# Kernel tuning notes

Measured on AMD Instinct MI355X. Metric: run time of the kernel, lower is better.

## Reference

```python
import jax, jax.numpy as jnp
import numpy as np

MAX_IT = 20
LAMBDA_ROF = 7.0
SIGMA = 1.0 / (7.0 * 0.01)
TAU = 0.01
THETA = 0.5
M, N = 4096, 4096


def _forward_weighted_gradient(x, w):
    # x: [1, M, N], w: [2, M, N] -> [2, M, N]
    x0 = x[0]
    gx = jnp.pad(x0[:, 1:] - x0[:, :-1], ((0, 0), (0, 1)))  # last col stays 0
    gy = jnp.pad(x0[1:, :] - x0[:-1, :], ((0, 1), (0, 0)))  # last row stays 0
    return jnp.stack([gx, gy]) * w


def _backward_weighted_divergence(y, w):
    # y, w: [2, M, N] -> [1, M, N]
    yw = w * y
    h, v = yw[0], yw[1]
    d_h = jnp.concatenate([h[:, :1], h[:, 1:-1] - h[:, :-2], -h[:, -2:-1]], axis=1)
    d_v = jnp.concatenate([v[:1, :], v[1:-1, :] - v[:-2, :], -v[-2:-1, :]], axis=0)
    return (d_h + d_v)[None]


def setup_inputs() -> dict:
    key = jax.random.key(0)
    k1, k2, k3 = jax.random.split(key, 3)
    img_obs = jax.random.uniform(k1, (1, M, N), dtype=jnp.float32)
    w = jax.random.uniform(k2, (2, M, N), dtype=jnp.float32)
    y0 = jax.random.uniform(k3, (2, M, N), dtype=jnp.float32)
    return {"img_obs": img_obs, "w": w, "y0": y0}


def reference(img_obs, w, y0):
    denom = 1.0 + LAMBDA_ROF * TAU

    def body(carry, _):
        x, x_tilde, y = carry
        # dual update + L-inf ball projection (prox == clip to [-1, 1])
        y = jnp.clip(y + SIGMA * _forward_weighted_gradient(x_tilde, w), -1.0, 1.0)
        x_old = x
        # primal update
        x = (x + TAU * _backward_weighted_divergence(y, w)
             + LAMBDA_ROF * TAU * img_obs) / denom
        # over-relaxation
        x_tilde = x + THETA * (x - x_old)
        return (x, x_tilde, y), None

    (x, x_tilde, y), _ = jax.lax.scan(body, (img_obs, img_obs, y0), None, length=MAX_IT)
    return x_tilde
```

## Files before the change

### kernel.cpp

```cpp
#include <hip/hip_runtime.h>


#define MM 4096
#define NN 4096
static constexpr size_t PP = (size_t)MM * NN;

static constexpr float SIGMA_F  = 14.285714285714286f;
static constexpr float TAU_F    = 0.01f;
static constexpr float THETA_F  = 0.5f;
static constexpr float LT_F     = 0.07f;
static constexpr float INV_DEN  = 1.0f / 1.07f;

typedef _Float16 h16;
typedef __attribute__((ext_vector_type(8))) _Float16 h16x8;
typedef __attribute__((ext_vector_type(4))) float f32x4;

__device__ __forceinline__ float clip1(float v) {
    return fminf(1.0f, fmaxf(-1.0f, v));
}

template<bool H>
__device__ __forceinline__ void ld8(const void* p, size_t idx, float* o) {
    if constexpr (H) {
        h16x8 v = *reinterpret_cast<const h16x8*>(reinterpret_cast<const h16*>(p) + idx);
        for (int e = 0; e < 8; ++e) o[e] = (float)v[e];
    } else {
        const float* q = reinterpret_cast<const float*>(p) + idx;
        f32x4 a = *reinterpret_cast<const f32x4*>(q);
        f32x4 b = *reinterpret_cast<const f32x4*>(q + 4);
        o[0]=a.x; o[1]=a.y; o[2]=a.z; o[3]=a.w;
        o[4]=b.x; o[5]=b.y; o[6]=b.z; o[7]=b.w;
    }
}
template<bool H>
__device__ __forceinline__ float ld1(const void* p, size_t idx) {
    if constexpr (H) return (float)reinterpret_cast<const h16*>(p)[idx];
    else             return reinterpret_cast<const float*>(p)[idx];
}

template<int XM, bool LAST, bool WH>
__global__ __launch_bounds__(256)
void fused_kernel(const void* __restrict__ xprev, const void* __restrict__ xcur,
                  const h16* __restrict__ yin, const void* __restrict__ w,
                  const float* __restrict__ img,
                  h16* __restrict__ xnext, h16* __restrict__ yout,
                  float* __restrict__ out)
{
    constexpr bool HP = (XM == 2);
    constexpr bool HC = (XM >= 1);
    const int i  = blockIdx.y * 4 + threadIdx.y;
    const int j0 = (blockIdx.x * 64 + threadIdx.x) * 8;
    const size_t idx = (size_t)i * NN + j0;
    const bool hasL = (j0 > 0);
    const bool hasR = (j0 + 8 < NN);
    const bool hasU = (i > 0);
    const bool hasD = (i < MM - 1);

    float xpC[8], xcC[8], xtC[8];
    ld8<HP>(xprev, idx, xpC);
    ld8<HC>(xcur,  idx, xcC);
    for (int e = 0; e < 8; ++e) xtC[e] = fmaf(THETA_F, xcC[e] - xpC[e], xcC[e]);

    float xtL = 0.f, xtR = 0.f;
    if (hasL) { float xp = ld1<HP>(xprev, idx-1), xc = ld1<HC>(xcur, idx-1);
                xtL = fmaf(THETA_F, xc - xp, xc); }
    if (hasR) { float xp = ld1<HP>(xprev, idx+8), xc = ld1<HC>(xcur, idx+8);
                xtR = fmaf(THETA_F, xc - xp, xc); }

    float xtU[8], xtD[8];
    if (hasU) {
        float xp[8], xc[8];
        ld8<HP>(xprev, idx - NN, xp);
        ld8<HC>(xcur,  idx - NN, xc);
        for (int e = 0; e < 8; ++e) xtU[e] = fmaf(THETA_F, xc[e] - xp[e], xc[e]);
    } else {
        for (int e = 0; e < 8; ++e) xtU[e] = 0.f;
    }
    if (hasD) {
        float xp[8], xc[8];
        ld8<HP>(xprev, idx + NN, xp);
        ld8<HC>(xcur,  idx + NN, xc);
        for (int e = 0; e < 8; ++e) xtD[e] = fmaf(THETA_F, xc[e] - xp[e], xc[e]);
    } else {
        for (int e = 0; e < 8; ++e) xtD[e] = 0.f;
    }

    float y0C[8], y1C[8], y1U[8];
    ld8<true>(yin, idx, y0C);
    ld8<true>(yin, PP + idx, y1C);
    float y0L = hasL ? ld1<true>(yin, idx - 1) : 0.f;
    if (hasU) {
        ld8<true>(yin, PP + idx - NN, y1U);
    } else {
        for (int e = 0; e < 8; ++e) y1U[e] = 0.f;
    }

    float w0C[8], w1C[8], w1U[8];
    ld8<WH>(w, idx, w0C);
    ld8<WH>(w, PP + idx, w1C);
    float w0L = hasL ? ld1<WH>(w, idx - 1) : 0.f;
    if (hasU) {
        ld8<WH>(w, PP + idx - NN, w1U);
    } else {
        for (int e = 0; e < 8; ++e) w1U[e] = 0.f;
    }

    float gv[8];
    ld8<false>(img, idx, gv);

    float y0n[8];
    for (int e = 0; e < 7; ++e)
        y0n[e] = clip1(fmaf(SIGMA_F * (xtC[e+1] - xtC[e]), w0C[e], y0C[e]));
    { float gx7 = hasR ? (xtR - xtC[7]) : 0.f;
      y0n[7] = clip1(fmaf(SIGMA_F * gx7, w0C[7], y0C[7])); }
    float y0nL = hasL ? clip1(fmaf(SIGMA_F * (xtC[0] - xtL), w0L, y0L)) : 0.f;

    float y1nC[8], y1nU[8];
    for (int e = 0; e < 8; ++e) {
        float gy = hasD ? (xtD[e] - xtC[e]) : 0.f;
        y1nC[e] = clip1(fmaf(SIGMA_F * gy, w1C[e], y1C[e]));
    }
    if (hasU) {
        for (int e = 0; e < 8; ++e)
            y1nU[e] = clip1(fmaf(SIGMA_F * (xtC[e] - xtU[e]), w1U[e], y1U[e]));
    } else {
        for (int e = 0; e < 8; ++e) y1nU[e] = 0.f;
    }

    float h[8];
    for (int e = 0; e < 8; ++e) h[e] = w0C[e] * y0n[e];
    const float hL = hasL ? w0L * y0nL : 0.f;
    float dh[8];
    dh[0] = h[0] - hL;
    for (int e = 1; e < 7; ++e) dh[e] = h[e] - h[e-1];
    dh[7] = (hasR ? h[7] : 0.f) - h[6];

    float dv[8];
    for (int e = 0; e < 8; ++e)
        dv[e] = (hasD ? w1C[e] * y1nC[e] : 0.f) - (hasU ? w1U[e] * y1nU[e] : 0.f);

    float xn[8];
    for (int e = 0; e < 8; ++e)
        xn[e] = (xcC[e] + TAU_F * (dh[e] + dv[e]) + LT_F * gv[e]) * INV_DEN;

    if constexpr (!LAST) {
        h16x8 s0, s1, sx;
        for (int e = 0; e < 8; ++e) {
            s0[e] = (h16)y0n[e];
            s1[e] = (h16)y1nC[e];
            sx[e] = (h16)xn[e];
        }
        *reinterpret_cast<h16x8*>(yout + idx)      = s0;
        *reinterpret_cast<h16x8*>(yout + PP + idx) = s1;
        *reinterpret_cast<h16x8*>(xnext + idx)     = sx;
    } else {
        float xt_[8];
        for (int e = 0; e < 8; ++e) xt_[e] = fmaf(THETA_F, xn[e] - xcC[e], xn[e]);
        f32x4 a, b;
        a.x = xt_[0]; a.y = xt_[1]; a.z = xt_[2]; a.w = xt_[3];
        b.x = xt_[4]; b.y = xt_[5]; b.z = xt_[6]; b.w = xt_[7];
        *reinterpret_cast<f32x4*>(out + idx)     = a;
        *reinterpret_cast<f32x4*>(out + idx + 4) = b;
    }
}

__global__ __launch_bounds__(256)
void cvt_f32_h16(const float* __restrict__ src, h16* __restrict__ dst) {
    const size_t t = (size_t)blockIdx.x * blockDim.x + threadIdx.x;
    const size_t idx = t * 8;
    f32x4 a = *reinterpret_cast<const f32x4*>(src + idx);
    f32x4 b = *reinterpret_cast<const f32x4*>(src + idx + 4);
    h16x8 v;
    v[0]=(h16)a.x; v[1]=(h16)a.y; v[2]=(h16)a.z; v[3]=(h16)a.w;
    v[4]=(h16)b.x; v[5]=(h16)b.y; v[6]=(h16)b.z; v[7]=(h16)b.w;
    *reinterpret_cast<h16x8*>(dst + idx) = v;
}

template<int XM, bool LAST>
static void launch_one(bool wh, dim3 g, dim3 b, hipStream_t s,
                       const void* xp, const void* xc, const h16* yin, const void* w,
                       const float* img, h16* xn, h16* yo, float* out) {
    if (wh) fused_kernel<XM, LAST, true ><<<g, b, 0, s>>>(xp, xc, yin, w, img, xn, yo, out);
    else    fused_kernel<XM, LAST, false><<<g, b, 0, s>>>(xp, xc, yin, w, img, xn, yo, out);
}

extern "C" void kernel_launch(void* const* d_in, const int* in_sizes, int n_in,
                              void* d_out, int out_size, void* d_ws, size_t ws_size,
                              hipStream_t stream) {
    const float* img = (const float*)d_in[0];
    const float* w   = (const float*)d_in[1];
    const float* y0  = (const float*)d_in[2];

    h16* base = (h16*)d_ws;
    h16* xb[3] = { base, base + PP, base + 2 * PP };
    h16* yA  = base + 3 * PP;
    h16* w_h = base + 5 * PP;
    h16* yB  = (h16*)d_out;

    const bool use_wh = (ws_size >= 7 * PP * sizeof(h16));

    {
        const int blocks = (int)(2 * PP / (8 * 256));
        cvt_f32_h16<<<blocks, 256, 0, stream>>>(y0, yB);
        if (use_wh) cvt_f32_h16<<<blocks, 256, 0, stream>>>(w, w_h);
    }
    const void* wp = use_wh ? (const void*)w_h : (const void*)w;

    const dim3 block(64, 4);
    const dim3 grid(NN / (64 * 8), MM / 4);
    const int MAX_IT = 20;

    for (int t = 0; t < MAX_IT; ++t) {
        const void* xp = (t <= 1) ? (const void*)img : (const void*)xb[(t - 2) % 3];
        const void* xc = (t == 0) ? (const void*)img : (const void*)xb[(t - 1) % 3];
        const h16* yin = (t % 2 == 0) ? yB : yA;
        h16* yout      = (t % 2 == 0) ? yA : yB;
        h16* xnext     = xb[t % 3];
        const bool last = (t == MAX_IT - 1);

        if (t == 0)
            launch_one<0, false>(use_wh, grid, block, stream, xp, xc, yin, wp, img, xnext, yout, (float*)d_out);
        else if (t == 1)
            launch_one<1, false>(use_wh, grid, block, stream, xp, xc, yin, wp, img, xnext, yout, (float*)d_out);
        else if (!last)
            launch_one<2, false>(use_wh, grid, block, stream, xp, xc, yin, wp, img, xnext, yout, (float*)d_out);
        else
            launch_one<2, true >(use_wh, grid, block, stream, xp, xc, yin, wp, img, xnext, yout, (float*)d_out);
    }
}
```

Measured before the change: 1.746 ms.

## Fuse two PDHG iterations per launch with shared-memory halo tiles

Replaces the one-iteration-per-launch stencil with a temporally blocked kernel. Each launch runs two primal-dual iterations on a 16x128 tile plus halo held in LDS, so the launch count drops from 20 to 10 and intermediate x/y traffic to global memory is roughly halved. The fp16 conversions of y0, w and img move into the first launch, and img can now be stored in fp16. Halo rows and columns are recomputed redundantly, and the larger LDS footprint and extra barriers may limit occupancy.

After: 1.706 ms. 1.02x faster.

```diff
diff --git a/kernel.cpp b/kernel.cpp
--- a/kernel.cpp
+++ b/kernel.cpp
@@ -15,173 +15,359 @@
 typedef __attribute__((ext_vector_type(8))) _Float16 h16x8;
 typedef __attribute__((ext_vector_type(4))) float f32x4;
 
+#define TR 16
+#define TC 128
+#define BR 20
+#define NSTRIP 18
+#define LSW 152
+
 __device__ __forceinline__ float clip1(float v) {
     return fminf(1.0f, fmaxf(-1.0f, v));
 }
 
 template<bool H>
-__device__ __forceinline__ void ld8(const void* p, size_t idx, float* o) {
+__device__ __forceinline__ void gld8(const void* __restrict__ p, long idx, bool ok, float* o) {
+    if (!ok) {
+        #pragma unroll
+        for (int e = 0; e < 8; ++e) o[e] = 0.f;
+        return;
+    }
     if constexpr (H) {
         h16x8 v = *reinterpret_cast<const h16x8*>(reinterpret_cast<const h16*>(p) + idx);
+        #pragma unroll
         for (int e = 0; e < 8; ++e) o[e] = (float)v[e];
     } else {
         const float* q = reinterpret_cast<const float*>(p) + idx;
         f32x4 a = *reinterpret_cast<const f32x4*>(q);
         f32x4 b = *reinterpret_cast<const f32x4*>(q + 4);
-        o[0]=a.x; o[1]=a.y; o[2]=a.z; o[3]=a.w;
-        o[4]=b.x; o[5]=b.y; o[6]=b.z; o[7]=b.w;
-    }
-}
+        o[0]=a.x;o[1]=a.y;o[2]=a.z;o[3]=a.w;o[4]=b.x;o[5]=b.y;o[6]=b.z;o[7]=b.w;
+    }
+}
+
 template<bool H>
-__device__ __forceinline__ float ld1(const void* p, size_t idx) {
+__device__ __forceinline__ float gld1(const void* __restrict__ p, long idx, bool ok) {
+    if (!ok) return 0.f;
     if constexpr (H) return (float)reinterpret_cast<const h16*>(p)[idx];
     else             return reinterpret_cast<const float*>(p)[idx];
 }
 
-template<int XM, bool LAST, bool WH>
-__global__ __launch_bounds__(256)
-void fused_kernel(const void* __restrict__ xprev, const void* __restrict__ xcur,
-                  const h16* __restrict__ yin, const void* __restrict__ w,
-                  const float* __restrict__ img,
-                  h16* __restrict__ xnext, h16* __restrict__ yout,
-                  float* __restrict__ out)
+__device__ __forceinline__ void lds8h(const h16* p, float* o) {
+    h16x8 v = *reinterpret_cast<const h16x8*>(p);
+    #pragma unroll
+    for (int e = 0; e < 8; ++e) o[e] = (float)v[e];
+}
+__device__ __forceinline__ void lds8f(const float* p, float* o) {
+    f32x4 a = *reinterpret_cast<const f32x4*>(p);
+    f32x4 b = *reinterpret_cast<const f32x4*>(p + 4);
+    o[0]=a.x;o[1]=a.y;o[2]=a.z;o[3]=a.w;o[4]=b.x;o[5]=b.y;o[6]=b.z;o[7]=b.w;
+}
+
+template<int MODE, bool WH, bool IH>
+__global__ __launch_bounds__(256, 4)
+void pd2(const h16* __restrict__ xprev, const h16* __restrict__ xcur,
+         const void* __restrict__ yin, const void* __restrict__ w,
+         const void* __restrict__ img,
+         h16* __restrict__ xo1, h16* __restrict__ xo2, h16* __restrict__ yo,
+         h16* __restrict__ w_h, h16* __restrict__ img_h,
+         float* __restrict__ out)
 {
-    constexpr bool HP = (XM == 2);
-    constexpr bool HC = (XM >= 1);
-    const int i  = blockIdx.y * 4 + threadIdx.y;
-    const int j0 = (blockIdx.x * 64 + threadIdx.x) * 8;
-    const size_t idx = (size_t)i * NN + j0;
-    const bool hasL = (j0 > 0);
-    const bool hasR = (j0 + 8 < NN);
-    const bool hasU = (i > 0);
-    const bool hasD = (i < MM - 1);
-
-    float xpC[8], xcC[8], xtC[8];
-    ld8<HP>(xprev, idx, xpC);
-    ld8<HC>(xcur,  idx, xcC);
-    for (int e = 0; e < 8; ++e) xtC[e] = fmaf(THETA_F, xcC[e] - xpC[e], xcC[e]);
-
-    float xtL = 0.f, xtR = 0.f;
-    if (hasL) { float xp = ld1<HP>(xprev, idx-1), xc = ld1<HC>(xcur, idx-1);
-                xtL = fmaf(THETA_F, xc - xp, xc); }
-    if (hasR) { float xp = ld1<HP>(xprev, idx+8), xc = ld1<HC>(xcur, idx+8);
-                xtR = fmaf(THETA_F, xc - xp, xc); }
-
-    float xtU[8], xtD[8];
-    if (hasU) {
-        float xp[8], xc[8];
-        ld8<HP>(xprev, idx - NN, xp);
-        ld8<HC>(xcur,  idx - NN, xc);
-        for (int e = 0; e < 8; ++e) xtU[e] = fmaf(THETA_F, xc[e] - xp[e], xc[e]);
-    } else {
-        for (int e = 0; e < 8; ++e) xtU[e] = 0.f;
-    }
-    if (hasD) {
-        float xp[8], xc[8];
-        ld8<HP>(xprev, idx + NN, xp);
-        ld8<HC>(xcur,  idx + NN, xc);
-        for (int e = 0; e < 8; ++e) xtD[e] = fmaf(THETA_F, xc[e] - xp[e], xc[e]);
-    } else {
-        for (int e = 0; e < 8; ++e) xtD[e] = 0.f;
-    }
-
-    float y0C[8], y1C[8], y1U[8];
-    ld8<true>(yin, idx, y0C);
-    ld8<true>(yin, PP + idx, y1C);
-    float y0L = hasL ? ld1<true>(yin, idx - 1) : 0.f;
-    if (hasU) {
-        ld8<true>(yin, PP + idx - NN, y1U);
-    } else {
-        for (int e = 0; e < 8; ++e) y1U[e] = 0.f;
-    }
-
-    float w0C[8], w1C[8], w1U[8];
-    ld8<WH>(w, idx, w0C);
-    ld8<WH>(w, PP + idx, w1C);
-    float w0L = hasL ? ld1<WH>(w, idx - 1) : 0.f;
-    if (hasU) {
-        ld8<WH>(w, PP + idx - NN, w1U);
-    } else {
-        for (int e = 0; e < 8; ++e) w1U[e] = 0.f;
-    }
-
-    float gv[8];
-    ld8<false>(img, idx, gv);
-
-    float y0n[8];
-    for (int e = 0; e < 7; ++e)
-        y0n[e] = clip1(fmaf(SIGMA_F * (xtC[e+1] - xtC[e]), w0C[e], y0C[e]));
-    { float gx7 = hasR ? (xtR - xtC[7]) : 0.f;
-      y0n[7] = clip1(fmaf(SIGMA_F * gx7, w0C[7], y0C[7])); }
-    float y0nL = hasL ? clip1(fmaf(SIGMA_F * (xtC[0] - xtL), w0L, y0L)) : 0.f;
-
-    float y1nC[8], y1nU[8];
-    for (int e = 0; e < 8; ++e) {
-        float gy = hasD ? (xtD[e] - xtC[e]) : 0.f;
-        y1nC[e] = clip1(fmaf(SIGMA_F * gy, w1C[e], y1C[e]));
-    }
-    if (hasU) {
-        for (int e = 0; e < 8; ++e)
-            y1nU[e] = clip1(fmaf(SIGMA_F * (xtC[e] - xtU[e]), w1U[e], y1U[e]));
-    } else {
-        for (int e = 0; e < 8; ++e) y1nU[e] = 0.f;
-    }
-
-    float h[8];
-    for (int e = 0; e < 8; ++e) h[e] = w0C[e] * y0n[e];
-    const float hL = hasL ? w0L * y0nL : 0.f;
-    float dh[8];
-    dh[0] = h[0] - hL;
-    for (int e = 1; e < 7; ++e) dh[e] = h[e] - h[e-1];
-    dh[7] = (hasR ? h[7] : 0.f) - h[6];
-
-    float dv[8];
-    for (int e = 0; e < 8; ++e)
-        dv[e] = (hasD ? w1C[e] * y1nC[e] : 0.f) - (hasU ? w1U[e] * y1nU[e] : 0.f);
-
-    float xn[8];
-    for (int e = 0; e < 8; ++e)
-        xn[e] = (xcC[e] + TAU_F * (dh[e] + dv[e]) + LT_F * gv[e]) * INV_DEN;
-
-    if constexpr (!LAST) {
-        h16x8 s0, s1, sx;
-        for (int e = 0; e < 8; ++e) {
-            s0[e] = (h16)y0n[e];
-            s1[e] = (h16)y1nC[e];
-            sx[e] = (h16)xn[e];
-        }
-        *reinterpret_cast<h16x8*>(yout + idx)      = s0;
-        *reinterpret_cast<h16x8*>(yout + PP + idx) = s1;
-        *reinterpret_cast<h16x8*>(xnext + idx)     = sx;
-    } else {
-        float xt_[8];
-        for (int e = 0; e < 8; ++e) xt_[e] = fmaf(THETA_F, xn[e] - xcC[e], xn[e]);
-        f32x4 a, b;
-        a.x = xt_[0]; a.y = xt_[1]; a.z = xt_[2]; a.w = xt_[3];
-        b.x = xt_[4]; b.y = xt_[5]; b.z = xt_[6]; b.w = xt_[7];
-        *reinterpret_cast<f32x4*>(out + idx)     = a;
-        *reinterpret_cast<f32x4*>(out + idx + 4) = b;
-    }
-}
-
-__global__ __launch_bounds__(256)
-void cvt_f32_h16(const float* __restrict__ src, h16* __restrict__ dst) {
-    const size_t t = (size_t)blockIdx.x * blockDim.x + threadIdx.x;
-    const size_t idx = t * 8;
-    f32x4 a = *reinterpret_cast<const f32x4*>(src + idx);
-    f32x4 b = *reinterpret_cast<const f32x4*>(src + idx + 4);
-    h16x8 v;
-    v[0]=(h16)a.x; v[1]=(h16)a.y; v[2]=(h16)a.z; v[3]=(h16)a.w;
-    v[4]=(h16)b.x; v[5]=(h16)b.y; v[6]=(h16)b.z; v[7]=(h16)b.w;
-    *reinterpret_cast<h16x8*>(dst + idx) = v;
-}
-
-template<int XM, bool LAST>
-static void launch_one(bool wh, dim3 g, dim3 b, hipStream_t s,
-                       const void* xp, const void* xc, const h16* yin, const void* w,
-                       const float* img, h16* xn, h16* yo, float* out) {
-    if (wh) fused_kernel<XM, LAST, true ><<<g, b, 0, s>>>(xp, xc, yin, w, img, xn, yo, out);
-    else    fused_kernel<XM, LAST, false><<<g, b, 0, s>>>(xp, xc, yin, w, img, xn, yo, out);
+    constexpr bool FIRST = (MODE == 0);
+    constexpr bool LAST  = (MODE == 2);
+    constexpr bool WRH = (!FIRST) && WH;
+    constexpr bool IRH = (!FIRST) && IH;
+
+    __shared__ float sXT[BR][LSW];
+    __shared__ h16   sX [BR][LSW];
+    __shared__ h16   sY0[BR][LSW];
+    __shared__ h16   sY1[BR][LSW];
+
+    const int tid = threadIdx.x;
+    const int bi0 = blockIdx.y * TR;
+    const int bj0 = blockIdx.x * TC;
+
+    for (int t = tid; t < BR * NSTRIP; t += 256) {
+        const int r = t / NSTRIP, s = t - r * NSTRIP;
+        const int gi = bi0 - 2 + r;
+        const int gj = bj0 - 8 + 8 * s;
+        const long idx = (long)gi * NN + gj;
+        const bool ok = (gi >= 0) & (gi < MM) & (gj >= 0) & (gj < NN);
+        const int l = 8 * s;
+        float xt8[8]; h16x8 xh;
+        if constexpr (FIRST) {
+            float v[8];
+            gld8<false>(img, idx, ok, v);
+            #pragma unroll
+            for (int e = 0; e < 8; ++e) { xt8[e] = v[e]; xh[e] = (h16)v[e]; }
+        } else {
+            float xp[8], xc[8];
+            gld8<true>(xprev, idx, ok, xp);
+            gld8<true>(xcur,  idx, ok, xc);
+            #pragma unroll
+            for (int e = 0; e < 8; ++e) {
+                xt8[e] = fmaf(THETA_F, xc[e] - xp[e], xc[e]);
+                xh[e]  = (h16)xc[e];
+            }
+        }
+        #pragma unroll
+        for (int e = 0; e < 8; ++e) sXT[r][l + e] = xt8[e];
+        *reinterpret_cast<h16x8*>(&sX[r][l]) = xh;
+    }
+    __syncthreads();
+
+    for (int t = tid; t < 19 * NSTRIP; t += 256) {
+        const int r = t / NSTRIP, s = t - r * NSTRIP;
+        const int gi = bi0 - 2 + r;
+        const int gj0 = bj0 - 8 + 8 * s;
+        const long idx = (long)gi * NN + gj0;
+        const bool ok = (gi >= 0) & (gi < MM) & (gj0 >= 0) & (gj0 < NN);
+        const int l = 8 * s;
+
+        float y0v[8], y1v[8], w0v[8], w1v[8];
+        gld8<!FIRST>(yin, idx, ok, y0v);
+        gld8<!FIRST>(yin, (long)PP + idx, ok, y1v);
+        gld8<WRH>(w, idx, ok, w0v);
+        gld8<WRH>(w, (long)PP + idx, ok, w1v);
+
+        float xtC[8], xtD[8];
+        lds8f(&sXT[r][l], xtC);
+        const float xtR = sXT[r][l + 8];
+        lds8f(&sXT[r + 1][l], xtD);
+
+        h16x8 y0s, y1s;
+        #pragma unroll
+        for (int e = 0; e < 8; ++e) {
+            const int gj = gj0 + e;
+            const float xtr = (e < 7) ? xtC[e + 1] : xtR;
+            const float gx = (gj < NN - 1) ? (xtr - xtC[e]) : 0.f;
+            const float gy = (gi < MM - 1) ? (xtD[e] - xtC[e]) : 0.f;
+            y0s[e] = (h16)clip1(fmaf(SIGMA_F * gx, w0v[e], y0v[e]));
+            y1s[e] = (h16)clip1(fmaf(SIGMA_F * gy, w1v[e], y1v[e]));
+        }
+        *reinterpret_cast<h16x8*>(&sY0[r][l]) = y0s;
+        *reinterpret_cast<h16x8*>(&sY1[r][l]) = y1s;
+
+        if constexpr (FIRST && WH) {
+            if (r >= 2 && r <= 17 && s >= 1 && s <= 16) {
+                h16x8 a, b;
+                #pragma unroll
+                for (int e = 0; e < 8; ++e) { a[e] = (h16)w0v[e]; b[e] = (h16)w1v[e]; }
+                *reinterpret_cast<h16x8*>(&w_h[idx]) = a;
+                *reinterpret_cast<h16x8*>(&w_h[PP + idx]) = b;
+            }
+        }
+    }
+    __syncthreads();
+
+    for (int t = tid; t < 18 * NSTRIP; t += 256) {
+        const int r = 1 + t / NSTRIP, s = t % NSTRIP;
+        const int gi = bi0 - 2 + r;
+        const int gj0 = bj0 - 8 + 8 * s;
+        const long idx = (long)gi * NN + gj0;
+        const bool ok  = (gi >= 0) & (gi < MM) & (gj0 >= 0) & (gj0 < NN);
+        const bool okU = (gi >= 1) & (gj0 >= 0) & (gj0 < NN);
+        const int l = 8 * s;
+
+        float y0C[8], y1C[8], y1U[8];
+        lds8h(&sY0[r][l], y0C);
+        lds8h(&sY1[r][l], y1C);
+        lds8h(&sY1[r - 1][l], y1U);
+        const int lm1 = (l > 0) ? (l - 1) : 0;
+        const float y0L = (float)sY0[r][lm1];
+
+        float w0C[8], w1C[8], w1U[8];
+        gld8<WRH>(w, idx, ok, w0C);
+        gld8<WRH>(w, (long)PP + idx, ok, w1C);
+        gld8<WRH>(w, (long)PP + idx - NN, okU, w1U);
+        const float w0L = gld1<WRH>(w, idx - 1, ok & (gj0 > 0));
+
+        float gim[8];
+        gld8<IRH>(img, idx, ok, gim);
+
+        float xc[8];
+        if constexpr (FIRST) {
+            #pragma unroll
+            for (int e = 0; e < 8; ++e) xc[e] = gim[e];
+        } else {
+            lds8h(&sX[r][l], xc);
+        }
+
+        float h[8];
+        #pragma unroll
+        for (int e = 0; e < 8; ++e) {
+            const int gj = gj0 + e;
+            h[e] = (gj < NN - 1) ? w0C[e] * y0C[e] : 0.f;
+        }
+        const float hL = w0L * y0L;
+        float dh[8];
+        dh[0] = h[0] - hL;
+        #pragma unroll
+        for (int e = 1; e < 8; ++e) dh[e] = h[e] - h[e - 1];
+
+        const bool notbot = (gi < MM - 1);
+        h16x8 xh; float xt1[8];
+        #pragma unroll
+        for (int e = 0; e < 8; ++e) {
+            const float vC = notbot ? w1C[e] * y1C[e] : 0.f;
+            const float vU = w1U[e] * y1U[e];
+            const float xv = (xc[e] + TAU_F * (dh[e] + vC - vU) + LT_F * gim[e]) * INV_DEN;
+            const h16 hh = (h16)xv;
+            const float xvh = (float)hh;
+            xh[e] = hh;
+            xt1[e] = fmaf(THETA_F, xvh - xc[e], xvh);
+        }
+        *reinterpret_cast<h16x8*>(&sX[r][l]) = xh;
+        #pragma unroll
+        for (int e = 0; e < 8; ++e) sXT[r][l + e] = xt1[e];
+
+        if constexpr (!LAST) {
+            if (r >= 2 && r <= 17 && s >= 1 && s <= 16)
+                *reinterpret_cast<h16x8*>(&xo1[idx]) = xh;
+        }
+        if constexpr (FIRST && IH) {
+            if (r >= 2 && r <= 17 && s >= 1 && s <= 16) {
+                h16x8 g8;
+                #pragma unroll
+                for (int e = 0; e < 8; ++e) g8[e] = (h16)gim[e];
+                *reinterpret_cast<h16x8*>(&img_h[idx]) = g8;
+            }
+        }
+    }
+    __syncthreads();
+
+    for (int t = tid; t < 17 * 17; t += 256) {
+        const int r = 1 + t / 17, s = t % 17;
+        const int gi = bi0 - 2 + r;
+        const int gj0 = bj0 - 8 + 8 * s;
+        const long idx = (long)gi * NN + gj0;
+        const bool ok = (gi >= 0) & (gi < MM) & (gj0 >= 0) & (gj0 < NN);
+        const int l = 8 * s;
+
+        float w0v[8], w1v[8];
+        gld8<WRH>(w, idx, ok, w0v);
+        gld8<WRH>(w, (long)PP + idx, ok, w1v);
+
+        float xtC[8], xtD[8];
+        lds8f(&sXT[r][l], xtC);
+        const float xtR = sXT[r][l + 8];
+        lds8f(&sXT[r + 1][l], xtD);
+
+        float y0p[8], y1p[8];
+        lds8h(&sY0[r][l], y0p);
+        lds8h(&sY1[r][l], y1p);
+
+        h16x8 y0s, y1s;
+        #pragma unroll
+        for (int e = 0; e < 8; ++e) {
+            const int gj = gj0 + e;
+            const float xtr = (e < 7) ? xtC[e + 1] : xtR;
+            const float gx = (gj < NN - 1) ? (xtr - xtC[e]) : 0.f;
+            const float gy = (gi < MM - 1) ? (xtD[e] - xtC[e]) : 0.f;
+            y0s[e] = (h16)clip1(fmaf(SIGMA_F * gx, w0v[e], y0p[e]));
+            y1s[e] = (h16)clip1(fmaf(SIGMA_F * gy, w1v[e], y1p[e]));
+        }
+        *reinterpret_cast<h16x8*>(&sY0[r][l]) = y0s;
+        *reinterpret_cast<h16x8*>(&sY1[r][l]) = y1s;
+        if constexpr (!LAST) {
+            if (r >= 2 && s >= 1) {
+                *reinterpret_cast<h16x8*>(&yo[idx]) = y0s;
+                *reinterpret_cast<h16x8*>(&yo[PP + idx]) = y1s;
+            }
+        }
+    }
+    __syncthreads();
+
+    {
+        const int r = 2 + (tid >> 4);
+        const int s = 1 + (tid & 15);
+        const int gi = bi0 - 2 + r;
+        const int gj0 = bj0 - 8 + 8 * s;
+        const long idx = (long)gi * NN + gj0;
+        const int l = 8 * s;
+
+        float y0C[8], y1C[8], y1U[8];
+        lds8h(&sY0[r][l], y0C);
+        lds8h(&sY1[r][l], y1C);
+        lds8h(&sY1[r - 1][l], y1U);
+        const float y0L = (float)sY0[r][l - 1];
+
+        float w0C[8], w1C[8], w1U[8];
+        gld8<WRH>(w, idx, true, w0C);
+        gld8<WRH>(w, (long)PP + idx, true, w1C);
+        gld8<WRH>(w, (long)PP + idx - NN, gi > 0, w1U);
+        const float w0L = gld1<WRH>(w, idx - 1, gj0 > 0);
+
+        float gim[8];
+        gld8<IRH>(img, idx, true, gim);
+
+        float xc1[8];
+        lds8h(&sX[r][l], xc1);
+
+        float h[8];
+        #pragma unroll
+        for (int e = 0; e < 8; ++e) {
+            const int gj = gj0 + e;
+            h[e] = (gj < NN - 1) ? w0C[e] * y0C[e] : 0.f;
+        }
+        const float hL = w0L * y0L;
+        float dh[8];
+        dh[0] = h[0] - hL;
+        #pragma unroll
+        for (int e = 1; e < 8; ++e) dh[e] = h[e] - h[e - 1];
+
+        const bool notbot = (gi < MM - 1);
+        if constexpr (!LAST) {
+            h16x8 xh;
+            #pragma unroll
+            for (int e = 0; e < 8; ++e) {
+                const float vC = notbot ? w1C[e] * y1C[e] : 0.f;
+                const float vU = w1U[e] * y1U[e];
+                const float xv = (xc1[e] + TAU_F * (dh[e] + vC - vU) + LT_F * gim[e]) * INV_DEN;
+                xh[e] = (h16)xv;
+            }
+            *reinterpret_cast<h16x8*>(&xo2[idx]) = xh;
+        } else {
+            float o[8];
+            #pragma unroll
+            for (int e = 0; e < 8; ++e) {
+                const float vC = notbot ? w1C[e] * y1C[e] : 0.f;
+                const float vU = w1U[e] * y1U[e];
+                const float xv = (xc1[e] + TAU_F * (dh[e] + vC - vU) + LT_F * gim[e]) * INV_DEN;
+                o[e] = fmaf(THETA_F, xv - xc1[e], xv);
+            }
+            f32x4 a, b;
+            a.x = o[0]; a.y = o[1]; a.z = o[2]; a.w = o[3];
+            b.x = o[4]; b.y = o[5]; b.z = o[6]; b.w = o[7];
+            *reinterpret_cast<f32x4*>(&out[idx]) = a;
+            *reinterpret_cast<f32x4*>(&out[idx + 4]) = b;
+        }
+    }
+}
+
+template<bool WH, bool IH>
+static void run_seq(hipStream_t s, const float* img, const float* w, const float* y0,
+                    h16* const* xb, h16* yA, h16* yB, h16* w_h, h16* img_h, float* out)
+{
+    const dim3 grid(NN / TC, MM / TR);
+    const dim3 block(256);
+    for (int k = 0; k < 10; ++k) {
+        const h16* xp = xb[(2 * k + 3) & 3];
+        const h16* xc = xb[(2 * k) & 3];
+        h16* xo1 = xb[(2 * k + 1) & 3];
+        h16* xo2 = xb[(2 * k + 2) & 3];
+        const void* yin = (k == 0) ? (const void*)y0
+                                   : ((k & 1) ? (const void*)yA : (const void*)yB);
+        h16* yo = (k & 1) ? yB : yA;
+        const void* wp = (k == 0) ? (const void*)w
+                                  : (WH ? (const void*)w_h : (const void*)w);
+        const void* ip = (k == 0) ? (const void*)img
+                                  : (IH ? (const void*)img_h : (const void*)img);
+        if (k == 0)
+            pd2<0, WH, IH><<<grid, block, 0, s>>>(xp, xc, yin, wp, ip, xo1, xo2, yo, w_h, img_h, out);
+        else if (k == 9)
+            pd2<2, WH, IH><<<grid, block, 0, s>>>(xp, xc, yin, wp, ip, xo1, xo2, yo, w_h, img_h, out);
+        else
+            pd2<1, WH, IH><<<grid, block, 0, s>>>(xp, xc, yin, wp, ip, xo1, xo2, yo, w_h, img_h, out);
+    }
 }
 
 extern "C" void kernel_launch(void* const* d_in, const int* in_sizes, int n_in,
@@ -192,39 +378,20 @@
     const float* y0  = (const float*)d_in[2];
 
     h16* base = (h16*)d_ws;
-    h16* xb[3] = { base, base + PP, base + 2 * PP };
-    h16* yA  = base + 3 * PP;
-    h16* w_h = base + 5 * PP;
-    h16* yB  = (h16*)d_out;
-
-    const bool use_wh = (ws_size >= 7 * PP * sizeof(h16));
-
-    {
-        const int blocks = (int)(2 * PP / (8 * 256));
-        cvt_f32_h16<<<blocks, 256, 0, stream>>>(y0, yB);
-        if (use_wh) cvt_f32_h16<<<blocks, 256, 0, stream>>>(w, w_h);
-    }
-    const void* wp = use_wh ? (const void*)w_h : (const void*)w;
-
-    const dim3 block(64, 4);
-    const dim3 grid(NN / (64 * 8), MM / 4);
-    const int MAX_IT = 20;
-
-    for (int t = 0; t < MAX_IT; ++t) {
-        const void* xp = (t <= 1) ? (const void*)img : (const void*)xb[(t - 2) % 3];
-        const void* xc = (t == 0) ? (const void*)img : (const void*)xb[(t - 1) % 3];
-        const h16* yin = (t % 2 == 0) ? yB : yA;
-        h16* yout      = (t % 2 == 0) ? yA : yB;
-        h16* xnext     = xb[t % 3];
-        const bool last = (t == MAX_IT - 1);
-
-        if (t == 0)
-            launch_one<0, false>(use_wh, grid, block, stream, xp, xc, yin, wp, img, xnext, yout, (float*)d_out);
-        else if (t == 1)
-            launch_one<1, false>(use_wh, grid, block, stream, xp, xc, yin, wp, img, xnext, yout, (float*)d_out);
-        else if (!last)
-            launch_one<2, false>(use_wh, grid, block, stream, xp, xc, yin, wp, img, xnext, yout, (float*)d_out);
-        else
-            launch_one<2, true >(use_wh, grid, block, stream, xp, xc, yin, wp, img, xnext, yout, (float*)d_out);
-    }
-}
+    h16* xb[4] = { base, base + PP, base + 2 * PP, base + 3 * PP };
+    h16* yA = base + 4 * PP;
+
+    const size_t planes = ws_size / (PP * sizeof(h16));
+    const bool WH = planes >= 8;
+    const bool IH = (planes >= 9) || (planes == 7);
+    h16* w_h   = WH ? base + 6 * PP : nullptr;
+    h16* img_h = IH ? (WH ? base + 8 * PP : base + 6 * PP) : nullptr;
+
+    h16* yB = (h16*)d_out;
+    float* out = (float*)d_out;
+
+    if (WH && IH)      run_seq<true,  true >(stream, img, w, y0, xb, yA, yB, w_h, img_h, out);
+    else if (WH)       run_seq<true,  false>(stream, img, w, y0, xb, yA, yB, w_h, img_h, out);
+    else if (IH)       run_seq<false, true >(stream, img, w, y0, xb, yA, yB, w_h, img_h, out);
+    else               run_seq<false, false>(stream, img, w, y0, xb, yA, yB, w_h, img_h, out);
+}
```
